# Kernel optimization log

Hardware: AMD Instinct MI355X
Metric: run time of the kernel (lower is better)

The kernel has to match this reference:

```python
import jax, jax.numpy as jnp
import numpy as np

B, T, C = 4, 2048, 1024
H = 16
D = C // H  # 64

def setup_inputs() -> dict:
    key = jax.random.key(0)
    k1, k2, k3, k4, k5 = jax.random.split(key, 5)
    s = 0.02
    return {
        "x": jax.random.normal(k1, (B, T, C), dtype=jnp.float32),
        "Wqkv": jax.random.normal(k2, (C, 3 * C), dtype=jnp.float32) * s,
        "bqkv": jnp.zeros((3 * C,), dtype=jnp.float32),
        "Wout": jax.random.normal(k3, (C, C), dtype=jnp.float32) * s,
        "bout": jnp.zeros((C,), dtype=jnp.float32),
    }

def reference(x, Wqkv, bqkv, Wout, bout):
    b, t, c = x.shape
    scale = D ** -0.5
    qkv = x @ Wqkv + bqkv                      # [B,T,3C]
    qkv = qkv.reshape(b, t, 3, H, D)
    q = qkv[:, :, 0].transpose(0, 2, 1, 3)     # [B,H,T,D]
    k = qkv[:, :, 1].transpose(0, 2, 1, 3)
    v = qkv[:, :, 2].transpose(0, 2, 1, 3)
    att = jnp.einsum('bhqd,bhkd->bhqk', q, k) * scale
    causal = jnp.tril(jnp.ones((t, t), dtype=bool))
    att = jnp.where(causal, att, -jnp.inf)
    att = jax.nn.softmax(att, axis=-1)
    y = jnp.einsum('bhqk,bhkd->bhqd', att, v)  # [B,H,T,D]
    y = y.transpose(0, 2, 1, 3).reshape(b, t, c)
    return y @ Wout + bout
```

## Files before the change

### kernel.cpp

```cpp
#include <hip/hip_runtime.h>
#include <hip/hip_bf16.h>


using f32x4 = __attribute__((ext_vector_type(4))) float;
using s16x8 = __attribute__((ext_vector_type(8))) short;
using s16x4 = __attribute__((ext_vector_type(4))) short;

#define MFMA16(a, b, c) __builtin_amdgcn_mfma_f32_16x16x32_bf16(a, b, c, 0, 0, 0)

__device__ __forceinline__ unsigned short f2bf(float f) {
    unsigned u = __builtin_bit_cast(unsigned, f);
    u += 0x7fffu + ((u >> 16) & 1u);
    return (unsigned short)(u >> 16);
}

__device__ __forceinline__ void gl_lds16(const void* g, void* l) {
    __builtin_amdgcn_global_load_lds(
        (const __attribute__((address_space(1))) void*)g,
        (__attribute__((address_space(3))) void*)l, 16, 0, 0);
}

__global__ __launch_bounds__(256) void cvt_x(const float* __restrict__ x,
                                             unsigned short* __restrict__ xb, int n4) {
    int i = blockIdx.x * 256 + threadIdx.x;
    if (i < n4) {
        f32x4 v = ((const f32x4*)x)[i];
        s16x4 o;
        o[0] = (short)f2bf(v[0]); o[1] = (short)f2bf(v[1]);
        o[2] = (short)f2bf(v[2]); o[3] = (short)f2bf(v[3]);
        ((s16x4*)xb)[i] = o;
    }
}

__global__ __launch_bounds__(256) void cvt_tr(const float* __restrict__ W,
                                              unsigned short* __restrict__ Wt,
                                              int R, int Cc) {
    __shared__ unsigned short tile[64][72];
    const int r0 = blockIdx.x * 64, c0 = blockIdx.y * 64;
    const int tid = threadIdx.x;
    const int r = tid >> 4, c4 = (tid & 15) * 4;
#pragma unroll
    for (int i = 0; i < 4; ++i) {
        f32x4 v = *(const f32x4*)(W + (size_t)(r0 + r + i * 16) * Cc + c0 + c4);
#pragma unroll
        for (int j = 0; j < 4; ++j) tile[r + i * 16][c4 + j] = f2bf(v[j]);
    }
    __syncthreads();
#pragma unroll
    for (int i = 0; i < 4; ++i) {
        s16x4 o;
#pragma unroll
        for (int j = 0; j < 4; ++j) o[j] = (short)tile[c4 + j][r + i * 16];
        *(s16x4*)(Wt + (size_t)(c0 + r + i * 16) * R + r0 + c4) = o;
    }
}

__global__ __launch_bounds__(256) void tr_v(const unsigned short* __restrict__ v,
                                            unsigned short* __restrict__ vt) {
    __shared__ unsigned short tile[64][72];
    const int t0 = blockIdx.x * 64;
    const int bh = blockIdx.y;
    const unsigned short* src = v + (size_t)bh * 131072;
    unsigned short* dst = vt + (size_t)bh * 131072;
    const int tid = threadIdx.x;
    const int r = tid >> 3, c = (tid & 7) * 8;
#pragma unroll
    for (int i = 0; i < 2; ++i)
        *(s16x8*)(&tile[r + i * 32][c]) =
            *(const s16x8*)(src + (size_t)(t0 + r + i * 32) * 64 + c);
    __syncthreads();
#pragma unroll
    for (int i = 0; i < 2; ++i) {
        s16x8 o;
#pragma unroll
        for (int j = 0; j < 8; ++j) o[j] = (short)tile[c + j][r + i * 32];
        *(s16x8*)(dst + (size_t)(r + i * 32) * 2048 + t0 + c) = o;
    }
}

template <int MODE>
__global__ __launch_bounds__(256) void gemm_bt(
    const unsigned short* __restrict__ A, const unsigned short* __restrict__ Bt,
    const float* __restrict__ bias,
    unsigned short* __restrict__ qp, unsigned short* __restrict__ kp,
    unsigned short* __restrict__ vp, float* __restrict__ outp,
    int M, int N, int K)
{
    __shared__ unsigned short As[128 * 32];
    __shared__ unsigned short Bs[128 * 32];
    const int tid  = threadIdx.x;
    const int lane = tid & 63, w = tid >> 6;
    const int wm = w >> 1, wn = w & 1;
    const int g = lane >> 4, li = lane & 15;
    const int m0 = blockIdx.x * 128, n0 = blockIdx.y * 128;
    const int srow = lane >> 2, sc = (lane & 3) * 8;

    f32x4 acc[4][4] = {};

    for (int k0 = 0; k0 < K; k0 += 32) {
        __syncthreads();
#pragma unroll
        for (int j = 0; j < 2; ++j) {
            const int rr = w * 32 + j * 16;
            gl_lds16(A  + (size_t)(m0 + rr + srow) * K + k0 + sc, As + rr * 32);
            gl_lds16(Bt + (size_t)(n0 + rr + srow) * K + k0 + sc, Bs + rr * 32);
        }
        __syncthreads();

        s16x8 af[4], bf[4];
#pragma unroll
        for (int i = 0; i < 4; ++i)
            af[i] = *(const s16x8*)(As + (wm * 64 + i * 16 + li) * 32 + g * 8);
#pragma unroll
        for (int i = 0; i < 4; ++i)
            bf[i] = *(const s16x8*)(Bs + (wn * 64 + i * 16 + li) * 32 + g * 8);
#pragma unroll
        for (int mi = 0; mi < 4; ++mi)
#pragma unroll
            for (int ni = 0; ni < 4; ++ni)
                acc[mi][ni] = MFMA16(af[mi], bf[ni], acc[mi][ni]);
    }

#pragma unroll
    for (int mi = 0; mi < 4; ++mi)
#pragma unroll
        for (int ni = 0; ni < 4; ++ni)
#pragma unroll
            for (int r = 0; r < 4; ++r) {
                const int m = m0 + wm * 64 + mi * 16 + g * 4 + r;
                const int n = n0 + wn * 64 + ni * 16 + li;
                float val = acc[mi][ni][r] + bias[n];
                if (MODE == 0) {
                    const int s = n >> 10, h = (n >> 6) & 15, d = n & 63;
                    const int b = m >> 11, tt = m & 2047;
                    if (s == 0) val *= 0.1803368801111143f;
                    unsigned short* dst = (s == 0) ? qp : (s == 1) ? kp : vp;
                    dst[((size_t)(b * 16 + h) * 2048 + tt) * 64 + d] = f2bf(val);
                } else {
                    outp[(size_t)m * N + n] = val;
                }
            }
}

__device__ __forceinline__ void stage_kv(
    const unsigned short* __restrict__ kb, const unsigned short* __restrict__ vtb,
    unsigned short* KsB, unsigned short* VsB, int kbase, int w, int lane)
{
    const int srow = lane >> 3;
    const int sw = ((lane & 7) ^ srow) * 8;
#pragma unroll
    for (int jj = 0; jj < 2; ++jj) {
        const int j = w * 2 + jj;
        const int row = j * 8 + srow;
        gl_lds16(kb  + (size_t)(kbase + row) * 64 + sw, KsB + j * 512);
        gl_lds16(vtb + (size_t)row * 2048 + kbase + sw, VsB + j * 512);
    }
}

__global__ __launch_bounds__(256) void attn_k(
    const unsigned short* __restrict__ qbuf,
    const unsigned short* __restrict__ kbuf,
    const unsigned short* __restrict__ vtbuf,
    unsigned short* __restrict__ ybuf)
{
    __shared__ unsigned short Ks[4096];
    __shared__ unsigned short Vs[4096];
    __shared__ unsigned short Ps[4][16][72];

    const int tid  = threadIdx.x;
    const int lane = tid & 63, w = tid >> 6;
    const int g = lane >> 4, li = lane & 15;

    const int id   = blockIdx.x;
    const int slot = id >> 3;
    const int bh   = (id & 7) * 8 + (slot & 7);
    const int bx   = slot >> 3;

    const unsigned short* qb  = qbuf  + (size_t)bh * 131072;
    const unsigned short* kb  = kbuf  + (size_t)bh * 131072;
    const unsigned short* vtb = vtbuf + (size_t)bh * 131072;
    const int b = bh >> 4, h = bh & 15;

    for (int half = 0; half < 2; ++half) {
        const int qt  = half ? (31 - bx) : bx;
        const int q0  = qt * 64;
        const int wq0 = q0 + w * 16;
        const int qrow = wq0 + li;

        const unsigned short* qr = qb + (size_t)qrow * 64 + g * 8;
        const s16x8 qf0 = *(const s16x8*)qr;
        const s16x8 qf1 = *(const s16x8*)(qr + 32);

        f32x4 O[4] = {};
        float m = -1e30f, l = 0.f;

        const int nkb = qt + 1;
        stage_kv(kb, vtb, Ks, Vs, 0, w, lane);
        asm volatile("s_waitcnt vmcnt(0)" ::: "memory");
        __syncthreads();

        for (int t = 0; t < nkb; ++t) {
            const int kbase = t * 64;

            f32x4 sT[4];
#pragma unroll
            for (int nf = 0; nf < 4; ++nf) {
                const int r = nf * 16 + li;
                s16x8 kf0 = *(const s16x8*)(Ks + r * 64 + ((g ^ (li & 7)) << 3));
                s16x8 kf1 = *(const s16x8*)(Ks + r * 64 + (((g + 4) ^ (li & 7)) << 3));
                f32x4 a = {};
                a = MFMA16(kf0, qf0, a);
                a = MFMA16(kf1, qf1, a);
                sT[nf] = a;
            }

            if (kbase + 63 > wq0) {
#pragma unroll
                for (int nf = 0; nf < 4; ++nf)
#pragma unroll
                    for (int r = 0; r < 4; ++r)
                        if (kbase + nf * 16 + g * 4 + r > qrow) sT[nf][r] = -1e30f;
            }

            float t0 = fmaxf(fmaxf(sT[0][0], sT[0][1]), sT[0][2]);
            float t1 = fmaxf(fmaxf(sT[0][3], sT[1][0]), sT[1][1]);
            float t2 = fmaxf(fmaxf(sT[1][2], sT[1][3]), sT[2][0]);
            float t3 = fmaxf(fmaxf(sT[2][1], sT[2][2]), sT[2][3]);
            float t4 = fmaxf(fmaxf(sT[3][0], sT[3][1]), sT[3][2]);
            float mx = fmaxf(fmaxf(t0, t1), t2);
            mx = fmaxf(fmaxf(mx, t3), fmaxf(t4, sT[3][3]));
            mx = fmaxf(mx, __shfl_xor(mx, 16));
            mx = fmaxf(mx, __shfl_xor(mx, 32));

            if (__any(mx > m + 8.f)) {
                const float mnew = fmaxf(m, mx);
                const float fac  = __builtin_amdgcn_exp2f(m - mnew);
                m = mnew;
                l *= fac;
                float facr[4];
#pragma unroll
                for (int r = 0; r < 4; ++r) facr[r] = __shfl(fac, g * 4 + r);
#pragma unroll
                for (int nf = 0; nf < 4; ++nf)
#pragma unroll
                    for (int r = 0; r < 4; ++r) O[nf][r] *= facr[r];
            }

            float rs = 0.f;
#pragma unroll
            for (int nf = 0; nf < 4; ++nf)
#pragma unroll
                for (int r = 0; r < 4; ++r) {
                    float p = __builtin_amdgcn_exp2f(sT[nf][r] - m);
                    sT[nf][r] = p;
                    rs += p;
                }
            rs += __shfl_xor(rs, 16);
            rs += __shfl_xor(rs, 32);
            l += rs;

#pragma unroll
            for (int nf = 0; nf < 4; ++nf) {
                unsigned pk0, pk1;
                asm("v_cvt_pk_bf16_f32 %0, %1, %2"
                    : "=v"(pk0) : "v"(sT[nf][0]), "v"(sT[nf][1]));
                asm("v_cvt_pk_bf16_f32 %0, %1, %2"
                    : "=v"(pk1) : "v"(sT[nf][2]), "v"(sT[nf][3]));
                uint2 pv; pv.x = pk0; pv.y = pk1;
                *(uint2*)(&Ps[w][li][nf * 16 + g * 4]) = pv;
            }

            const s16x8 pf0 = *(const s16x8*)(&Ps[w][li][g * 8]);
            const s16x8 pf1 = *(const s16x8*)(&Ps[w][li][32 + g * 8]);

#pragma unroll
            for (int nf = 0; nf < 4; ++nf) {
                const int d = nf * 16 + li;
                s16x8 vf0 = *(const s16x8*)(Vs + d * 64 + ((g ^ (li & 7)) << 3));
                s16x8 vf1 = *(const s16x8*)(Vs + d * 64 + (((g + 4) ^ (li & 7)) << 3));
                O[nf] = MFMA16(pf0, vf0, O[nf]);
                O[nf] = MFMA16(pf1, vf1, O[nf]);
            }

            __syncthreads();
            if (t + 1 < nkb)
                stage_kv(kb, vtb, Ks, Vs, kbase + 64, w, lane);
            asm volatile("s_waitcnt vmcnt(0)" ::: "memory");
            __syncthreads();
        }

        const float linv = __builtin_amdgcn_rcpf(l);
        float lr[4];
#pragma unroll
        for (int r = 0; r < 4; ++r) lr[r] = __shfl(linv, g * 4 + r);

#pragma unroll
        for (int nf = 0; nf < 4; ++nf)
#pragma unroll
            for (int r = 0; r < 4; ++r) {
                const int row = wq0 + g * 4 + r;
                const int d = nf * 16 + li;
                ybuf[((size_t)(b * 2048 + row)) * 1024 + h * 64 + d] =
                    f2bf(O[nf][r] * lr[r]);
            }
    }
}

extern "C" void kernel_launch(void* const* d_in, const int* in_sizes, int n_in,
                              void* d_out, int out_size, void* d_ws, size_t ws_size,
                              hipStream_t stream)
{
    const float* x    = (const float*)d_in[0];
    const float* Wqkv = (const float*)d_in[1];
    const float* bqkv = (const float*)d_in[2];
    const float* Wout = (const float*)d_in[3];
    const float* bout = (const float*)d_in[4];

    unsigned short* ws0 = (unsigned short*)d_ws;
    unsigned short* ws1 = ws0 + (size_t)8388608;
    unsigned short* ws2 = ws0 + (size_t)2 * 8388608;
    unsigned short* ws3 = ws0 + (size_t)3 * 8388608;

    unsigned short* xbf   = (unsigned short*)d_out;
    unsigned short* WqkvT = xbf + (size_t)8388608;

    cvt_x<<<8192, 256, 0, stream>>>(x, xbf, 2097152);
    cvt_tr<<<dim3(16, 48), 256, 0, stream>>>(Wqkv, WqkvT, 1024, 3072);
    gemm_bt<0><<<dim3(64, 24), 256, 0, stream>>>(
        xbf, WqkvT, bqkv, ws0, ws1, ws3, nullptr, 8192, 3072, 1024);
    tr_v<<<dim3(32, 64), 256, 0, stream>>>(ws3, ws2);
    attn_k<<<1024, 256, 0, stream>>>(ws0, ws1, ws2, ws3);
    cvt_tr<<<dim3(16, 16), 256, 0, stream>>>(Wout, ws0, 1024, 1024);
    gemm_bt<1><<<dim3(64, 8), 256, 0, stream>>>(
        ws3, ws0, bout, nullptr, nullptr, nullptr, (float*)d_out, 8192, 1024, 1024);
}
```

Measured before the change: 194.4 us.

## Fuse V transpose into QKV GEMM epilogue and co-process paired query tiles

Measured after the change: 178.1 us. 8.4% less time.

```diff
diff --git a/kernel.cpp b/kernel.cpp
--- a/kernel.cpp
+++ b/kernel.cpp
@@ -55,35 +55,12 @@
     }
 }
 
-__global__ __launch_bounds__(256) void tr_v(const unsigned short* __restrict__ v,
-                                            unsigned short* __restrict__ vt) {
-    __shared__ unsigned short tile[64][72];
-    const int t0 = blockIdx.x * 64;
-    const int bh = blockIdx.y;
-    const unsigned short* src = v + (size_t)bh * 131072;
-    unsigned short* dst = vt + (size_t)bh * 131072;
-    const int tid = threadIdx.x;
-    const int r = tid >> 3, c = (tid & 7) * 8;
-#pragma unroll
-    for (int i = 0; i < 2; ++i)
-        *(s16x8*)(&tile[r + i * 32][c]) =
-            *(const s16x8*)(src + (size_t)(t0 + r + i * 32) * 64 + c);
-    __syncthreads();
-#pragma unroll
-    for (int i = 0; i < 2; ++i) {
-        s16x8 o;
-#pragma unroll
-        for (int j = 0; j < 8; ++j) o[j] = (short)tile[c + j][r + i * 32];
-        *(s16x8*)(dst + (size_t)(r + i * 32) * 2048 + t0 + c) = o;
-    }
-}
-
 template <int MODE>
 __global__ __launch_bounds__(256) void gemm_bt(
     const unsigned short* __restrict__ A, const unsigned short* __restrict__ Bt,
     const float* __restrict__ bias,
     unsigned short* __restrict__ qp, unsigned short* __restrict__ kp,
-    unsigned short* __restrict__ vp, float* __restrict__ outp,
+    unsigned short* __restrict__ vtp, float* __restrict__ outp,
     int M, int N, int K)
 {
     __shared__ unsigned short As[128 * 32];
@@ -122,24 +99,39 @@
     }
 
 #pragma unroll
-    for (int mi = 0; mi < 4; ++mi)
-#pragma unroll
-        for (int ni = 0; ni < 4; ++ni)
-#pragma unroll
-            for (int r = 0; r < 4; ++r) {
-                const int m = m0 + wm * 64 + mi * 16 + g * 4 + r;
-                const int n = n0 + wn * 64 + ni * 16 + li;
-                float val = acc[mi][ni][r] + bias[n];
-                if (MODE == 0) {
-                    const int s = n >> 10, h = (n >> 6) & 15, d = n & 63;
-                    const int b = m >> 11, tt = m & 2047;
-                    if (s == 0) val *= 0.1803368801111143f;
-                    unsigned short* dst = (s == 0) ? qp : (s == 1) ? kp : vp;
-                    dst[((size_t)(b * 16 + h) * 2048 + tt) * 64 + d] = f2bf(val);
+    for (int ni = 0; ni < 4; ++ni) {
+        const int n = n0 + wn * 64 + ni * 16 + li;
+        const float bv = bias[n];
+        const int s = n >> 10, h = (n >> 6) & 15, d = n & 63;
+#pragma unroll
+        for (int mi = 0; mi < 4; ++mi) {
+            const int mB = m0 + wm * 64 + mi * 16 + g * 4;
+            float v0 = acc[mi][ni][0] + bv, v1 = acc[mi][ni][1] + bv;
+            float v2 = acc[mi][ni][2] + bv, v3 = acc[mi][ni][3] + bv;
+            if (MODE == 0) {
+                const int b = mB >> 11, tt = mB & 2047;
+                if (s == 2) {
+                    unsigned pk01, pk23;
+                    asm("v_cvt_pk_bf16_f32 %0, %1, %2" : "=v"(pk01) : "v"(v0), "v"(v1));
+                    asm("v_cvt_pk_bf16_f32 %0, %1, %2" : "=v"(pk23) : "v"(v2), "v"(v3));
+                    unsigned short* dst = vtp + ((size_t)(b * 16 + h) * 64 + d) * 2048 + tt;
+                    *(unsigned*)dst = pk01;
+                    *(unsigned*)(dst + 2) = pk23;
                 } else {
-                    outp[(size_t)m * N + n] = val;
+                    const float sc2 = (s == 0) ? 0.1803368801111143f : 1.0f;
+                    unsigned short* dst =
+                        ((s == 0) ? qp : kp) + ((size_t)(b * 16 + h) * 2048 + tt) * 64 + d;
+                    dst[0]   = f2bf(v0 * sc2);
+                    dst[64]  = f2bf(v1 * sc2);
+                    dst[128] = f2bf(v2 * sc2);
+                    dst[192] = f2bf(v3 * sc2);
                 }
+            } else {
+                float* dst = outp + (size_t)mB * N + n;
+                dst[0] = v0; dst[N] = v1; dst[2 * N] = v2; dst[3 * N] = v3;
             }
+        }
+    }
 }
 
 __device__ __forceinline__ void stage_kv(
@@ -157,7 +149,84 @@
     }
 }
 
-__global__ __launch_bounds__(256) void attn_k(
+__device__ __forceinline__ void qk_softmax(
+    const unsigned short* Ks, const s16x8 qf0, const s16x8 qf1,
+    f32x4 (&O)[4], float& m, float& l,
+    unsigned short (*Psw)[72], s16x8& pf0, s16x8& pf1,
+    int kbase, int wq0, int qrow, int g, int li)
+{
+    f32x4 sT[4];
+    __builtin_amdgcn_s_setprio(1);
+#pragma unroll
+    for (int nf = 0; nf < 4; ++nf) {
+        const int r = nf * 16 + li;
+        s16x8 kf0 = *(const s16x8*)(Ks + r * 64 + ((g ^ (li & 7)) << 3));
+        s16x8 kf1 = *(const s16x8*)(Ks + r * 64 + (((g + 4) ^ (li & 7)) << 3));
+        f32x4 a = {};
+        a = MFMA16(kf0, qf0, a);
+        a = MFMA16(kf1, qf1, a);
+        sT[nf] = a;
+    }
+    __builtin_amdgcn_s_setprio(0);
+
+    if (kbase + 63 > wq0) {
+#pragma unroll
+        for (int nf = 0; nf < 4; ++nf)
+#pragma unroll
+            for (int r = 0; r < 4; ++r)
+                if (kbase + nf * 16 + g * 4 + r > qrow) sT[nf][r] = -1e30f;
+    }
+
+    float t0 = fmaxf(fmaxf(sT[0][0], sT[0][1]), sT[0][2]);
+    float t1 = fmaxf(fmaxf(sT[0][3], sT[1][0]), sT[1][1]);
+    float t2 = fmaxf(fmaxf(sT[1][2], sT[1][3]), sT[2][0]);
+    float t3 = fmaxf(fmaxf(sT[2][1], sT[2][2]), sT[2][3]);
+    float t4 = fmaxf(fmaxf(sT[3][0], sT[3][1]), sT[3][2]);
+    float mx = fmaxf(fmaxf(t0, t1), t2);
+    mx = fmaxf(fmaxf(mx, t3), fmaxf(t4, sT[3][3]));
+    mx = fmaxf(mx, __shfl_xor(mx, 16));
+    mx = fmaxf(mx, __shfl_xor(mx, 32));
+
+    if (__any(mx > m + 8.f)) {
+        const float mnew = fmaxf(m, mx);
+        const float fac  = __builtin_amdgcn_exp2f(m - mnew);
+        m = mnew;
+        l *= fac;
+        float facr[4];
+#pragma unroll
+        for (int r = 0; r < 4; ++r) facr[r] = __shfl(fac, g * 4 + r);
+#pragma unroll
+        for (int nf = 0; nf < 4; ++nf)
+#pragma unroll
+            for (int r = 0; r < 4; ++r) O[nf][r] *= facr[r];
+    }
+
+    float rs = 0.f;
+#pragma unroll
+    for (int nf = 0; nf < 4; ++nf)
+#pragma unroll
+        for (int r = 0; r < 4; ++r) {
+            float p = __builtin_amdgcn_exp2f(sT[nf][r] - m);
+            sT[nf][r] = p;
+            rs += p;
+        }
+    rs += __shfl_xor(rs, 16);
+    rs += __shfl_xor(rs, 32);
+    l += rs;
+
+#pragma unroll
+    for (int nf = 0; nf < 4; ++nf) {
+        unsigned pk0, pk1;
+        asm("v_cvt_pk_bf16_f32 %0, %1, %2" : "=v"(pk0) : "v"(sT[nf][0]), "v"(sT[nf][1]));
+        asm("v_cvt_pk_bf16_f32 %0, %1, %2" : "=v"(pk1) : "v"(sT[nf][2]), "v"(sT[nf][3]));
+        uint2 pv; pv.x = pk0; pv.y = pk1;
+        *(uint2*)(&Psw[li][nf * 16 + g * 4]) = pv;
+    }
+    pf0 = *(const s16x8*)(&Psw[li][g * 8]);
+    pf1 = *(const s16x8*)(&Psw[li][32 + g * 8]);
+}
+
+__global__ __launch_bounds__(256, 4) void attn_k(
     const unsigned short* __restrict__ qbuf,
     const unsigned short* __restrict__ kbuf,
     const unsigned short* __restrict__ vtbuf,
@@ -165,7 +234,8 @@
 {
     __shared__ unsigned short Ks[4096];
     __shared__ unsigned short Vs[4096];
-    __shared__ unsigned short Ps[4][16][72];
+    __shared__ unsigned short PsA[4][16][72];
+    __shared__ unsigned short PsB[4][16][72];
 
     const int tid  = threadIdx.x;
     const int lane = tid & 63, w = tid >> 6;
@@ -175,133 +245,91 @@
     const int slot = id >> 3;
     const int bh   = (id & 7) * 8 + (slot & 7);
     const int bx   = slot >> 3;
+    const int qtA  = 31 - bx, qtB = bx;
 
     const unsigned short* qb  = qbuf  + (size_t)bh * 131072;
     const unsigned short* kb  = kbuf  + (size_t)bh * 131072;
     const unsigned short* vtb = vtbuf + (size_t)bh * 131072;
     const int b = bh >> 4, h = bh & 15;
 
-    for (int half = 0; half < 2; ++half) {
-        const int qt  = half ? (31 - bx) : bx;
-        const int q0  = qt * 64;
-        const int wq0 = q0 + w * 16;
-        const int qrow = wq0 + li;
-
-        const unsigned short* qr = qb + (size_t)qrow * 64 + g * 8;
-        const s16x8 qf0 = *(const s16x8*)qr;
-        const s16x8 qf1 = *(const s16x8*)(qr + 32);
-
-        f32x4 O[4] = {};
-        float m = -1e30f, l = 0.f;
-
-        const int nkb = qt + 1;
-        stage_kv(kb, vtb, Ks, Vs, 0, w, lane);
-        asm volatile("s_waitcnt vmcnt(0)" ::: "memory");
-        __syncthreads();
-
-        for (int t = 0; t < nkb; ++t) {
-            const int kbase = t * 64;
-
-            f32x4 sT[4];
-#pragma unroll
-            for (int nf = 0; nf < 4; ++nf) {
-                const int r = nf * 16 + li;
-                s16x8 kf0 = *(const s16x8*)(Ks + r * 64 + ((g ^ (li & 7)) << 3));
-                s16x8 kf1 = *(const s16x8*)(Ks + r * 64 + (((g + 4) ^ (li & 7)) << 3));
-                f32x4 a = {};
-                a = MFMA16(kf0, qf0, a);
-                a = MFMA16(kf1, qf1, a);
-                sT[nf] = a;
+    const int wqA = qtA * 64 + w * 16, qrowA = wqA + li;
+    const int wqB = qtB * 64 + w * 16, qrowB = wqB + li;
+
+    const unsigned short* qrA = qb + (size_t)qrowA * 64 + g * 8;
+    const s16x8 qfA0 = *(const s16x8*)qrA;
+    const s16x8 qfA1 = *(const s16x8*)(qrA + 32);
+    const unsigned short* qrB = qb + (size_t)qrowB * 64 + g * 8;
+    const s16x8 qfB0 = *(const s16x8*)qrB;
+    const s16x8 qfB1 = *(const s16x8*)(qrB + 32);
+
+    f32x4 OA[4] = {}, OB[4] = {};
+    float mA = -1e30f, lA = 0.f, mB = -1e30f, lB = 0.f;
+
+    const int nkb = qtA + 1;
+    stage_kv(kb, vtb, Ks, Vs, 0, w, lane);
+    asm volatile("s_waitcnt vmcnt(0)" ::: "memory");
+    __syncthreads();
+
+    for (int t = 0; t < nkb; ++t) {
+        const int kbase = t * 64;
+        const bool actB = (t <= qtB);
+
+        s16x8 pfA0, pfA1, pfB0, pfB1;
+        qk_softmax(Ks, qfA0, qfA1, OA, mA, lA, &PsA[w][0], pfA0, pfA1,
+                   kbase, wqA, qrowA, g, li);
+        if (actB)
+            qk_softmax(Ks, qfB0, qfB1, OB, mB, lB, &PsB[w][0], pfB0, pfB1,
+                       kbase, wqB, qrowB, g, li);
+
+        __builtin_amdgcn_s_setprio(1);
+#pragma unroll
+        for (int nf = 0; nf < 4; ++nf) {
+            const int d = nf * 16 + li;
+            s16x8 vf0 = *(const s16x8*)(Vs + d * 64 + ((g ^ (li & 7)) << 3));
+            s16x8 vf1 = *(const s16x8*)(Vs + d * 64 + (((g + 4) ^ (li & 7)) << 3));
+            OA[nf] = MFMA16(pfA0, vf0, OA[nf]);
+            OA[nf] = MFMA16(pfA1, vf1, OA[nf]);
+            if (actB) {
+                OB[nf] = MFMA16(pfB0, vf0, OB[nf]);
+                OB[nf] = MFMA16(pfB1, vf1, OB[nf]);
             }
-
-            if (kbase + 63 > wq0) {
-#pragma unroll
-                for (int nf = 0; nf < 4; ++nf)
-#pragma unroll
-                    for (int r = 0; r < 4; ++r)
-                        if (kbase + nf * 16 + g * 4 + r > qrow) sT[nf][r] = -1e30f;
-            }
-
-            float t0 = fmaxf(fmaxf(sT[0][0], sT[0][1]), sT[0][2]);
-            float t1 = fmaxf(fmaxf(sT[0][3], sT[1][0]), sT[1][1]);
-            float t2 = fmaxf(fmaxf(sT[1][2], sT[1][3]), sT[2][0]);
-            float t3 = fmaxf(fmaxf(sT[2][1], sT[2][2]), sT[2][3]);
-            float t4 = fmaxf(fmaxf(sT[3][0], sT[3][1]), sT[3][2]);
-            float mx = fmaxf(fmaxf(t0, t1), t2);
-            mx = fmaxf(fmaxf(mx, t3), fmaxf(t4, sT[3][3]));
-            mx = fmaxf(mx, __shfl_xor(mx, 16));
-            mx = fmaxf(mx, __shfl_xor(mx, 32));
-
-            if (__any(mx > m + 8.f)) {
-                const float mnew = fmaxf(m, mx);
-                const float fac  = __builtin_amdgcn_exp2f(m - mnew);
-                m = mnew;
-                l *= fac;
-                float facr[4];
-#pragma unroll
-                for (int r = 0; r < 4; ++r) facr[r] = __shfl(fac, g * 4 + r);
-#pragma unroll
-                for (int nf = 0; nf < 4; ++nf)
-#pragma unroll
-                    for (int r = 0; r < 4; ++r) O[nf][r] *= facr[r];
-            }
-
-            float rs = 0.f;
-#pragma unroll
-            for (int nf = 0; nf < 4; ++nf)
-#pragma unroll
-                for (int r = 0; r < 4; ++r) {
-                    float p = __builtin_amdgcn_exp2f(sT[nf][r] - m);
-                    sT[nf][r] = p;
-                    rs += p;
-                }
-            rs += __shfl_xor(rs, 16);
-            rs += __shfl_xor(rs, 32);
-            l += rs;
-
-#pragma unroll
-            for (int nf = 0; nf < 4; ++nf) {
-                unsigned pk0, pk1;
-                asm("v_cvt_pk_bf16_f32 %0, %1, %2"
-                    : "=v"(pk0) : "v"(sT[nf][0]), "v"(sT[nf][1]));
-                asm("v_cvt_pk_bf16_f32 %0, %1, %2"
-                    : "=v"(pk1) : "v"(sT[nf][2]), "v"(sT[nf][3]));
-                uint2 pv; pv.x = pk0; pv.y = pk1;
-                *(uint2*)(&Ps[w][li][nf * 16 + g * 4]) = pv;
-            }
-
-            const s16x8 pf0 = *(const s16x8*)(&Ps[w][li][g * 8]);
-            const s16x8 pf1 = *(const s16x8*)(&Ps[w][li][32 + g * 8]);
-
-#pragma unroll
-            for (int nf = 0; nf < 4; ++nf) {
-                const int d = nf * 16 + li;
-                s16x8 vf0 = *(const s16x8*)(Vs + d * 64 + ((g ^ (li & 7)) << 3));
-                s16x8 vf1 = *(const s16x8*)(Vs + d * 64 + (((g + 4) ^ (li & 7)) << 3));
-                O[nf] = MFMA16(pf0, vf0, O[nf]);
-                O[nf] = MFMA16(pf1, vf1, O[nf]);
-            }
-
+        }
+        __builtin_amdgcn_s_setprio(0);
+
+        if (t + 1 < nkb) {
             __syncthreads();
-            if (t + 1 < nkb)
-                stage_kv(kb, vtb, Ks, Vs, kbase + 64, w, lane);
+            stage_kv(kb, vtb, Ks, Vs, kbase + 64, w, lane);
             asm volatile("s_waitcnt vmcnt(0)" ::: "memory");
             __syncthreads();
         }
-
-        const float linv = __builtin_amdgcn_rcpf(l);
+    }
+
+    {
+        const float linv = __builtin_amdgcn_rcpf(lA);
         float lr[4];
 #pragma unroll
         for (int r = 0; r < 4; ++r) lr[r] = __shfl(linv, g * 4 + r);
-
 #pragma unroll
         for (int nf = 0; nf < 4; ++nf)
 #pragma unroll
             for (int r = 0; r < 4; ++r) {
-                const int row = wq0 + g * 4 + r;
-                const int d = nf * 16 + li;
-                ybuf[((size_t)(b * 2048 + row)) * 1024 + h * 64 + d] =
-                    f2bf(O[nf][r] * lr[r]);
+                const int row = wqA + g * 4 + r;
+                ybuf[((size_t)(b * 2048 + row)) * 1024 + h * 64 + nf * 16 + li] =
+                    f2bf(OA[nf][r] * lr[r]);
+            }
+    }
+    {
+        const float linv = __builtin_amdgcn_rcpf(lB);
+        float lr[4];
+#pragma unroll
+        for (int r = 0; r < 4; ++r) lr[r] = __shfl(linv, g * 4 + r);
+#pragma unroll
+        for (int nf = 0; nf < 4; ++nf)
+#pragma unroll
+            for (int r = 0; r < 4; ++r) {
+                const int row = wqB + g * 4 + r;
+                ybuf[((size_t)(b * 2048 + row)) * 1024 + h * 64 + nf * 16 + li] =
+                    f2bf(OB[nf][r] * lr[r]);
             }
     }
 }
@@ -327,8 +355,7 @@
     cvt_x<<<8192, 256, 0, stream>>>(x, xbf, 2097152);
     cvt_tr<<<dim3(16, 48), 256, 0, stream>>>(Wqkv, WqkvT, 1024, 3072);
     gemm_bt<0><<<dim3(64, 24), 256, 0, stream>>>(
-        xbf, WqkvT, bqkv, ws0, ws1, ws3, nullptr, 8192, 3072, 1024);
-    tr_v<<<dim3(32, 64), 256, 0, stream>>>(ws3, ws2);
+        xbf, WqkvT, bqkv, ws0, ws1, ws2, nullptr, 8192, 3072, 1024);
     attn_k<<<1024, 256, 0, stream>>>(ws0, ws1, ws2, ws3);
     cvt_tr<<<dim3(16, 16), 256, 0, stream>>>(Wout, ws0, 1024, 1024);
     gemm_bt<1><<<dim3(64, 8), 256, 0, stream>>>(
```
